# Kernel tuning notes

Hardware: AMD Instinct MI355X
Metric: run time of the kernel (lower is better)

The kernel has to match this reference:

```python
import jax, jax.numpy as jnp
import numpy as np

N = 50000
E = 800000
IN_C = 512
HID_C = 128
OUT_C = 16


def setup_inputs() -> dict:
    key = jax.random.key(0)
    k1, k2, k3, k4, k5 = jax.random.split(key, 5)
    x = jax.random.normal(k1, (N, IN_C), dtype=jnp.float32)
    edge_index = jax.random.randint(k2, (2, E), 0, N, dtype=jnp.int64)
    # GCNConv.lin: Linear(in, hid, bias=False); conv bias zero-init but give random for grad coverage
    W1 = jax.random.normal(k3, (HID_C, IN_C), dtype=jnp.float32) / np.sqrt(IN_C)
    b1 = jnp.zeros((HID_C,), dtype=jnp.float32)
    # GCNNet.fc: Linear(hid, out)
    W2 = jax.random.normal(k4, (OUT_C, HID_C), dtype=jnp.float32) / np.sqrt(HID_C)
    b2 = jax.random.normal(k5, (OUT_C,), dtype=jnp.float32) * 0.01
    return {"x": x, "edge_index": edge_index, "W1": W1, "b1": b1, "W2": W2, "b2": b2}


def reference(x, edge_index, W1, b1, W2, b2):
    # Dropout(p=0.5) is identity in eval mode.
    row, col = edge_index[0], edge_index[1]
    h = x @ W1.T                                    # [N, HID_C]
    deg = jax.ops.segment_sum(jnp.ones((E,), dtype=h.dtype), col, num_segments=N)
    # NOTE: source uses deg.pow(0.5) (sqrt, not inv-sqrt) — faithful to the code.
    d = jnp.sqrt(deg)
    norm = d[row] * d[col]                          # [E]
    msg = norm[:, None] * h[row]                    # gather + scale, [E, HID_C]
    agg = jax.ops.segment_sum(msg, col, num_segments=N)  # scatter-add, [N, HID_C]
    conv_out = agg + b1                             # [N, HID_C]
    return conv_out @ W2.T + b2                     # [N, OUT_C]
```

## Files before the change

kernel.cpp:

```cpp
#include <hip/hip_runtime.h>
#include <hip/hip_bf16.h>
#include <hip/hip_fp16.h>

#define IN_C 512
#define HID_C 128
#define OUT_C 16
#define STILE 8192
#define SSH  13
#define KCH_H 32

typedef float    f32x4 __attribute__((ext_vector_type(4)));
typedef float    f32x2 __attribute__((ext_vector_type(2)));
typedef int      i32x4 __attribute__((ext_vector_type(4)));
typedef _Float16 h16x2 __attribute__((ext_vector_type(2)));

__device__ inline void pk_atomic_add_f16(h16x2* addr, h16x2 val) {
#if __has_builtin(__builtin_amdgcn_global_atomic_fadd_v2f16)
    __builtin_amdgcn_global_atomic_fadd_v2f16(addr, val);
#else
    unsigned int* ap = (unsigned int*)addr;
    unsigned int old = *ap, assumed;
    do {
        assumed = old;
        h16x2 cur = __builtin_bit_cast(h16x2, assumed);
        h16x2 nv = cur + val;
        old = atomicCAS(ap, assumed, __builtin_bit_cast(unsigned int, nv));
    } while (old != assumed);
#endif
}

__global__ __launch_bounds__(256) void prep_hist_kernel(
        const float* __restrict__ W1, const float* __restrict__ b1,
        const float* __restrict__ W2, const float* __restrict__ b2,
        float* __restrict__ Wc, float* __restrict__ cconst,
        const int* __restrict__ ei, int* __restrict__ phist,
        unsigned int* __restrict__ agg32, int E, int nhist, int aggWords) {
    __shared__ int h[STILE];
    if (blockIdx.x < 32) {
        int idx = blockIdx.x * 256 + threadIdx.x;
        int o = idx >> 9;
        int k = idx & 511;
        float s = 0.f;
#pragma unroll 8
        for (int hh = 0; hh < HID_C; ++hh)
            s = fmaf(W2[o * HID_C + hh], W1[hh * IN_C + k], s);
        Wc[o * IN_C + k] = s;
        return;
    }
    if (blockIdx.x == 32) {
        if (threadIdx.x < OUT_C) {
            int o = threadIdx.x;
            float s = b2[o];
            for (int hh = 0; hh < HID_C; ++hh)
                s = fmaf(b1[hh], W2[o * HID_C + hh], s);
            cconst[o] = s;
        }
        return;
    }
    if (blockIdx.x >= 33 + nhist) {
        int i = (blockIdx.x - 33 - nhist) * 256 + threadIdx.x;
        if (i < aggWords) agg32[i] = 0u;
        return;
    }
    const int hb = blockIdx.x - 33;
    const int st = hb / KCH_H;
    const int k = hb - st * KCH_H;
    for (int i = threadIdx.x; i < STILE; i += 256) h[i] = 0;
    __syncthreads();

    const int chunk = (((E + KCH_H - 1) / KCH_H) + 3) & ~3;
    const int beg = k * chunk;
    const int end = min(E, beg + chunk);
    const int* cols = ei + E;

    const int nv = (end > beg) ? ((end - beg) >> 2) : 0;
    const i32x4* cv = (const i32x4*)(cols + beg);
    for (int i = threadIdx.x; i < nv; i += 256) {
        i32x4 c = cv[i];
#pragma unroll
        for (int j = 0; j < 4; ++j) {
            int cj = c[j];
            if ((cj >> SSH) == st) atomicAdd(&h[cj & (STILE - 1)], 1);
        }
    }
    for (int e = beg + (nv << 2) + threadIdx.x; e < end; e += 256) {
        int cj = cols[e];
        if ((cj >> SSH) == st) atomicAdd(&h[cj & (STILE - 1)], 1);
    }
    __syncthreads();
    int* outp = phist + (size_t)hb * STILE;
    for (int i = threadIdx.x; i < STILE; i += 256) outp[i] = h[i];
}

__global__ __launch_bounds__(256) void h2_kernel(const float* __restrict__ x,
                                                 const float* __restrict__ WcG,
                                                 const int* __restrict__ phist,
                                                 float* __restrict__ dsq,
                                                 _Float16* __restrict__ h2h, int N) {
    __shared__ float wl[16 * IN_C];
    for (int i = threadIdx.x; i < (16 * IN_C) / 4; i += 256)
        ((f32x4*)wl)[i] = ((const f32x4*)WcG)[i];
    __syncthreads();

    const int lane = threadIdx.x & 63;
    const int wid = (blockIdx.x * 256 + threadIdx.x) >> 6;
    const int nw  = (gridDim.x * 256) >> 6;

    for (int r0 = wid * 4; r0 < N; r0 += nw * 4) {
        const int rmax = min(4, N - r0);

        const int rr_d = lane >> 4;
        const int rd = min(r0 + rr_d, N - 1);
        const int std = rd >> SSH, id = rd & (STILE - 1);
        const int kd = lane & 15;
        const int* pb = phist + ((size_t)std * KCH_H) * STILE + id;
        int deg = pb[(size_t)kd * STILE] + pb[(size_t)(kd + 16) * STILE];
        deg += __shfl_xor(deg, 1, 64);
        deg += __shfl_xor(deg, 2, 64);
        deg += __shfl_xor(deg, 4, 64);
        deg += __shfl_xor(deg, 8, 64);
        const float dsq_r = sqrtf((float)deg);
        if (kd == 0 && rr_d < rmax) dsq[r0 + rr_d] = dsq_r;

        f32x4 a0[4], a1[4];
#pragma unroll
        for (int rr = 0; rr < 4; ++rr) {
            int r = r0 + (rr < rmax ? rr : 0);
            a0[rr] = *(const f32x4*)(x + (size_t)r * IN_C + 4 * lane);
            a1[rr] = *(const f32x4*)(x + (size_t)r * IN_C + 256 + 4 * lane);
        }
        float p[4][16];
#pragma unroll
        for (int oo = 0; oo < 16; ++oo) {
            f32x4 w0 = *(const f32x4*)(wl + oo * IN_C + 4 * lane);
            f32x4 w1 = *(const f32x4*)(wl + oo * IN_C + 256 + 4 * lane);
#pragma unroll
            for (int rr = 0; rr < 4; ++rr) {
                float s = a0[rr].x * w0.x;
                s = fmaf(a0[rr].y, w0.y, s);
                s = fmaf(a0[rr].z, w0.z, s);
                s = fmaf(a0[rr].w, w0.w, s);
                s = fmaf(a1[rr].x, w1.x, s);
                s = fmaf(a1[rr].y, w1.y, s);
                s = fmaf(a1[rr].z, w1.z, s);
                s = fmaf(a1[rr].w, w1.w, s);
                p[rr][oo] = s;
            }
        }
        float v[4];
#pragma unroll
        for (int rr = 0; rr < 4; ++rr) {
#define RSTEP(MASK, HALF)                                              \
            {                                                          \
                const bool hi = (lane & MASK) != 0;                    \
                _Pragma("unroll")                                      \
                for (int ii = 0; ii < HALF; ++ii) {                    \
                    float send = hi ? p[rr][ii] : p[rr][ii + HALF];    \
                    float recv = __shfl_xor(send, MASK, 64);           \
                    float keep = hi ? p[rr][ii + HALF] : p[rr][ii];    \
                    p[rr][ii] = keep + recv;                           \
                }                                                      \
            }
            RSTEP(1, 8)
            RSTEP(2, 4)
            RSTEP(4, 2)
            RSTEP(8, 1)
#undef RSTEP
            v[rr] = p[rr][0];
        }
        const bool h16 = (lane & 16) != 0;
        float sA = h16 ? v[0] : v[1];
        float mA = (h16 ? v[1] : v[0]) + __shfl_xor(sA, 16, 64);
        float sB = h16 ? v[2] : v[3];
        float mB = (h16 ? v[3] : v[2]) + __shfl_xor(sB, 16, 64);
        const bool h32 = (lane & 32) != 0;
        float sC = h32 ? mA : mB;
        float f  = (h32 ? mB : mA) + __shfl_xor(sC, 32, 64);
        const int qq = lane >> 4, jj = lane & 15;
        const int oo = ((jj & 1) << 3) | ((jj & 2) << 1) | ((jj & 4) >> 1) | ((jj & 8) >> 3);
        if (qq < rmax) {
            int r = r0 + qq;
            h2h[(size_t)r * OUT_C + oo] = (_Float16)(f * dsq_r);
        }
    }
}

__global__ __launch_bounds__(256) void edge_kernel(const int* __restrict__ ei,
                                                   const _Float16* __restrict__ h2h,
                                                   h16x2* __restrict__ agg, int E) {
    int t = blockIdx.x * 256 + threadIdx.x;
    int e = t >> 3;
    if (e >= E) return;
    int op = t & 7;
    int r = ei[e];
    int c = ei[E + e];
    h16x2 h = *(const h16x2*)(h2h + (size_t)r * OUT_C + (op << 1));
    pk_atomic_add_f16(&agg[(size_t)c * 8 + op], h);
}

__global__ void final_kernel(const h16x2* __restrict__ agg, const float* __restrict__ dsq,
                             const float* __restrict__ cconst, float* __restrict__ out,
                             int words) {
    int i = blockIdx.x * 256 + threadIdx.x;
    if (i >= words) return;
    int n = i >> 3;
    int o = (i & 7) << 1;
    h16x2 a = agg[i];
    float d = dsq[n];
    f32x2 r;
    r.x = fmaf(d, (float)a.x, cconst[o]);
    r.y = fmaf(d, (float)a.y, cconst[o + 1]);
    *(f32x2*)(out + ((size_t)i << 1)) = r;
}

extern "C" void kernel_launch(void* const* d_in, const int* in_sizes, int n_in,
                              void* d_out, int out_size, void* d_ws, size_t ws_size,
                              hipStream_t stream) {
    const float* x  = (const float*)d_in[0];
    const int*   ei = (const int*)d_in[1];
    const float* W1 = (const float*)d_in[2];
    const float* b1 = (const float*)d_in[3];
    const float* W2 = (const float*)d_in[4];
    const float* b2 = (const float*)d_in[5];
    float* out = (float*)d_out;

    const int N = in_sizes[0] / IN_C;
    const int E = in_sizes[1] / 2;
    const int ST = (N + STILE - 1) / STILE;
    const int nhist = ST * KCH_H;
    const int aggWords = (N * OUT_C) / 2;

    float* ws     = (float*)d_ws;
    float* Wc     = ws;
    float* cconst = ws + 16 * IN_C;
    float* dsq    = cconst + 16;
    _Float16* h2h = (_Float16*)(dsq + N);
    int*   phist  = (int*)((unsigned int*)(dsq + N) + 8 * (size_t)N);
    unsigned int* agg32 = (unsigned int*)(phist + (size_t)ST * KCH_H * STILE);
    h16x2* agg = (h16x2*)agg32;

    const int zblocks = (aggWords + 255) / 256;
    hipLaunchKernelGGL(prep_hist_kernel, dim3(33 + nhist + zblocks), dim3(256), 0, stream,
                       W1, b1, W2, b2, Wc, cconst, ei, phist, agg32, E, nhist, aggWords);
    hipLaunchKernelGGL(h2_kernel, dim3(1024), dim3(256), 0, stream, x, Wc, phist, dsq, h2h, N);
    hipLaunchKernelGGL(edge_kernel, dim3((E * 8 + 255) / 256), dim3(256), 0, stream,
                       ei, h2h, agg, E);
    hipLaunchKernelGGL(final_kernel, dim3((aggWords + 255) / 256), dim3(256), 0, stream,
                       agg, dsq, cconst, out, aggWords);
}
```

Measured before the change: 90.84 us.

## Software-pipeline x row loads in h2 kernel with two rows per wave iteration

The h2 projection kernel now processes two rows per wave iteration instead of four and prefetches the next iteration's x rows into registers while computing the current ones. The goal is to hide global-load latency on the memory-bound x stream through register double buffering. The degree lookup is restructured to one load per lane over 32 histogram chunks. Each iteration has less arithmetic per load and one extra shuffle stage, and the final store uses only half the lanes.

```diff
diff --git a/kernel.cpp b/kernel.cpp
--- a/kernel.cpp
+++ b/kernel.cpp
@@ -105,54 +105,79 @@
     const int lane = threadIdx.x & 63;
     const int wid = (blockIdx.x * 256 + threadIdx.x) >> 6;
     const int nw  = (gridDim.x * 256) >> 6;
-
-    for (int r0 = wid * 4; r0 < N; r0 += nw * 4) {
-        const int rmax = min(4, N - r0);
-
-        const int rr_d = lane >> 4;
+    const int stride = nw * 2;
+
+    int r0 = wid * 2;
+    if (r0 >= N) return;
+
+    f32x4 a0c0, a1c0, a0c1, a1c1;
+    {
+        int ra = r0, rb = min(r0 + 1, N - 1);
+        a0c0 = *(const f32x4*)(x + (size_t)ra * IN_C + 4 * lane);
+        a1c0 = *(const f32x4*)(x + (size_t)ra * IN_C + 256 + 4 * lane);
+        a0c1 = *(const f32x4*)(x + (size_t)rb * IN_C + 4 * lane);
+        a1c1 = *(const f32x4*)(x + (size_t)rb * IN_C + 256 + 4 * lane);
+    }
+
+    while (r0 < N) {
+        const int rnext = r0 + stride;
+        f32x4 a0n0, a1n0, a0n1, a1n1;
+        if (rnext < N) {
+            int ra = rnext, rb = min(rnext + 1, N - 1);
+            a0n0 = *(const f32x4*)(x + (size_t)ra * IN_C + 4 * lane);
+            a1n0 = *(const f32x4*)(x + (size_t)ra * IN_C + 256 + 4 * lane);
+            a0n1 = *(const f32x4*)(x + (size_t)rb * IN_C + 4 * lane);
+            a1n1 = *(const f32x4*)(x + (size_t)rb * IN_C + 256 + 4 * lane);
+        }
+        const int rmax = min(2, N - r0);
+
+        const int rr_d = lane >> 5;
         const int rd = min(r0 + rr_d, N - 1);
-        const int std = rd >> SSH, id = rd & (STILE - 1);
-        const int kd = lane & 15;
-        const int* pb = phist + ((size_t)std * KCH_H) * STILE + id;
-        int deg = pb[(size_t)kd * STILE] + pb[(size_t)(kd + 16) * STILE];
+        const int std_ = rd >> SSH, id_ = rd & (STILE - 1);
+        const int kd = lane & 31;
+        int deg = phist[((size_t)std_ * KCH_H + kd) * STILE + id_];
         deg += __shfl_xor(deg, 1, 64);
         deg += __shfl_xor(deg, 2, 64);
         deg += __shfl_xor(deg, 4, 64);
         deg += __shfl_xor(deg, 8, 64);
+        deg += __shfl_xor(deg, 16, 64);
         const float dsq_r = sqrtf((float)deg);
         if (kd == 0 && rr_d < rmax) dsq[r0 + rr_d] = dsq_r;
-
-        f32x4 a0[4], a1[4];
-#pragma unroll
-        for (int rr = 0; rr < 4; ++rr) {
-            int r = r0 + (rr < rmax ? rr : 0);
-            a0[rr] = *(const f32x4*)(x + (size_t)r * IN_C + 4 * lane);
-            a1[rr] = *(const f32x4*)(x + (size_t)r * IN_C + 256 + 4 * lane);
-        }
-        float p[4][16];
+        const float dsq_o = __shfl_xor(dsq_r, 32, 64);
+
+        float p[2][16];
 #pragma unroll
         for (int oo = 0; oo < 16; ++oo) {
             f32x4 w0 = *(const f32x4*)(wl + oo * IN_C + 4 * lane);
             f32x4 w1 = *(const f32x4*)(wl + oo * IN_C + 256 + 4 * lane);
-#pragma unroll
-            for (int rr = 0; rr < 4; ++rr) {
-                float s = a0[rr].x * w0.x;
-                s = fmaf(a0[rr].y, w0.y, s);
-                s = fmaf(a0[rr].z, w0.z, s);
-                s = fmaf(a0[rr].w, w0.w, s);
-                s = fmaf(a1[rr].x, w1.x, s);
-                s = fmaf(a1[rr].y, w1.y, s);
-                s = fmaf(a1[rr].z, w1.z, s);
-                s = fmaf(a1[rr].w, w1.w, s);
-                p[rr][oo] = s;
+            {
+                float s = a0c0.x * w0.x;
+                s = fmaf(a0c0.y, w0.y, s);
+                s = fmaf(a0c0.z, w0.z, s);
+                s = fmaf(a0c0.w, w0.w, s);
+                s = fmaf(a1c0.x, w1.x, s);
+                s = fmaf(a1c0.y, w1.y, s);
+                s = fmaf(a1c0.z, w1.z, s);
+                s = fmaf(a1c0.w, w1.w, s);
+                p[0][oo] = s;
             }
-        }
-        float v[4];
-#pragma unroll
-        for (int rr = 0; rr < 4; ++rr) {
+            {
+                float s = a0c1.x * w0.x;
+                s = fmaf(a0c1.y, w0.y, s);
+                s = fmaf(a0c1.z, w0.z, s);
+                s = fmaf(a0c1.w, w0.w, s);
+                s = fmaf(a1c1.x, w1.x, s);
+                s = fmaf(a1c1.y, w1.y, s);
+                s = fmaf(a1c1.z, w1.z, s);
+                s = fmaf(a1c1.w, w1.w, s);
+                p[1][oo] = s;
+            }
+        }
 #define RSTEP(MASK, HALF)                                              \
-            {                                                          \
-                const bool hi = (lane & MASK) != 0;                    \
+        {                                                              \
+            const bool hi = (lane & MASK) != 0;                        \
+            _Pragma("unroll")                                          \
+            for (int rr = 0; rr < 2; ++rr) {                           \
                 _Pragma("unroll")                                      \
                 for (int ii = 0; ii < HALF; ++ii) {                    \
                     float send = hi ? p[rr][ii] : p[rr][ii + HALF];    \
@@ -160,28 +185,29 @@
                     float keep = hi ? p[rr][ii + HALF] : p[rr][ii];    \
                     p[rr][ii] = keep + recv;                           \
                 }                                                      \
+            }                                                          \
+        }
+        RSTEP(1, 8)
+        RSTEP(2, 4)
+        RSTEP(4, 2)
+        RSTEP(8, 1)
+#undef RSTEP
+        const float v0 = p[0][0], v1 = p[1][0];
+        const bool h16 = (lane & 16) != 0;
+        float sA = h16 ? v0 : v1;
+        float mA = (h16 ? v1 : v0) + __shfl_xor(sA, 16, 64);
+        float f  = mA + __shfl_xor(mA, 32, 64);
+        if (lane < 32) {
+            int rsel = (lane >> 4) & 1;
+            if (rsel < rmax) {
+                const int jj = lane & 15;
+                const int oo = ((jj & 1) << 3) | ((jj & 2) << 1) | ((jj & 4) >> 1) | ((jj & 8) >> 3);
+                const float d = (lane & 16) ? dsq_o : dsq_r;
+                h2h[(size_t)(r0 + rsel) * OUT_C + oo] = (_Float16)(f * d);
             }
-            RSTEP(1, 8)
-            RSTEP(2, 4)
-            RSTEP(4, 2)
-            RSTEP(8, 1)
-#undef RSTEP
-            v[rr] = p[rr][0];
-        }
-        const bool h16 = (lane & 16) != 0;
-        float sA = h16 ? v[0] : v[1];
-        float mA = (h16 ? v[1] : v[0]) + __shfl_xor(sA, 16, 64);
-        float sB = h16 ? v[2] : v[3];
-        float mB = (h16 ? v[3] : v[2]) + __shfl_xor(sB, 16, 64);
-        const bool h32 = (lane & 32) != 0;
-        float sC = h32 ? mA : mB;
-        float f  = (h32 ? mB : mA) + __shfl_xor(sC, 32, 64);
-        const int qq = lane >> 4, jj = lane & 15;
-        const int oo = ((jj & 1) << 3) | ((jj & 2) << 1) | ((jj & 4) >> 1) | ((jj & 8) >> 3);
-        if (qq < rmax) {
-            int r = r0 + qq;
-            h2h[(size_t)r * OUT_C + oo] = (_Float16)(f * dsq_r);
-        }
+        }
+        r0 = rnext;
+        a0c0 = a0n0; a1c0 = a1n0; a0c1 = a0n1; a1c1 = a1n1;
     }
 }
 
```

After: 93.13 us. 2.5% more time.

## Replicate fp16 aggregation buffer across block groups to reduce atomic contention

Applied to the files above, without the earlier changes.

Splits the edge scatter-add across 8 replicated fp16 accumulation buffers, one per contiguous group of edge blocks, and sums the replicas in the final kernel. This aims to spread atomic traffic across more addresses and improve L2 atomic throughput, and it also keeps fp16 partial sums smaller, which may help precision. In exchange it costs 8x more zero-initialisation work and 8x more reads in the final kernel, plus a larger workspace. The h2 kernel grid is also halved.

```diff
diff --git a/kernel.cpp b/kernel.cpp
--- a/kernel.cpp
+++ b/kernel.cpp
@@ -8,6 +8,7 @@
 #define STILE 8192
 #define SSH  13
 #define KCH_H 32
+#define NREP 8
 
 typedef float    f32x4 __attribute__((ext_vector_type(4)));
 typedef float    f32x2 __attribute__((ext_vector_type(2)));
@@ -34,7 +35,7 @@
         const float* __restrict__ W2, const float* __restrict__ b2,
         float* __restrict__ Wc, float* __restrict__ cconst,
         const int* __restrict__ ei, int* __restrict__ phist,
-        unsigned int* __restrict__ agg32, int E, int nhist, int aggWords) {
+        unsigned int* __restrict__ agg32, int E, int nhist, int zeroWords) {
     __shared__ int h[STILE];
     if (blockIdx.x < 32) {
         int idx = blockIdx.x * 256 + threadIdx.x;
@@ -59,7 +60,7 @@
     }
     if (blockIdx.x >= 33 + nhist) {
         int i = (blockIdx.x - 33 - nhist) * 256 + threadIdx.x;
-        if (i < aggWords) agg32[i] = 0u;
+        if (i < zeroWords) agg32[i] = 0u;
         return;
     }
     const int hb = blockIdx.x - 33;
@@ -111,9 +112,9 @@
 
         const int rr_d = lane >> 4;
         const int rd = min(r0 + rr_d, N - 1);
-        const int std = rd >> SSH, id = rd & (STILE - 1);
+        const int std_ = rd >> SSH, id_ = rd & (STILE - 1);
         const int kd = lane & 15;
-        const int* pb = phist + ((size_t)std * KCH_H) * STILE + id;
+        const int* pb = phist + ((size_t)std_ * KCH_H) * STILE + id_;
         int deg = pb[(size_t)kd * STILE] + pb[(size_t)(kd + 16) * STILE];
         deg += __shfl_xor(deg, 1, 64);
         deg += __shfl_xor(deg, 2, 64);
@@ -187,7 +188,9 @@
 
 __global__ __launch_bounds__(256) void edge_kernel(const int* __restrict__ ei,
                                                    const _Float16* __restrict__ h2h,
-                                                   h16x2* __restrict__ agg, int E) {
+                                                   h16x2* __restrict__ agg,
+                                                   int E, int aggWords, int repDiv) {
+    h16x2* aggR = agg + (size_t)(blockIdx.x / repDiv) * aggWords;
     int t = blockIdx.x * 256 + threadIdx.x;
     int e = t >> 3;
     if (e >= E) return;
@@ -195,21 +198,27 @@
     int r = ei[e];
     int c = ei[E + e];
     h16x2 h = *(const h16x2*)(h2h + (size_t)r * OUT_C + (op << 1));
-    pk_atomic_add_f16(&agg[(size_t)c * 8 + op], h);
+    pk_atomic_add_f16(&aggR[(size_t)c * 8 + op], h);
 }
 
 __global__ void final_kernel(const h16x2* __restrict__ agg, const float* __restrict__ dsq,
                              const float* __restrict__ cconst, float* __restrict__ out,
-                             int words) {
+                             int words, int aggWords) {
     int i = blockIdx.x * 256 + threadIdx.x;
     if (i >= words) return;
     int n = i >> 3;
     int o = (i & 7) << 1;
-    h16x2 a = agg[i];
+    float sx = 0.f, sy = 0.f;
+#pragma unroll
+    for (int rep = 0; rep < NREP; ++rep) {
+        h16x2 a = agg[(size_t)rep * aggWords + i];
+        sx += (float)a.x;
+        sy += (float)a.y;
+    }
     float d = dsq[n];
     f32x2 r;
-    r.x = fmaf(d, (float)a.x, cconst[o]);
-    r.y = fmaf(d, (float)a.y, cconst[o + 1]);
+    r.x = fmaf(d, sx, cconst[o]);
+    r.y = fmaf(d, sy, cconst[o + 1]);
     *(f32x2*)(out + ((size_t)i << 1)) = r;
 }
 
@@ -229,6 +238,7 @@
     const int ST = (N + STILE - 1) / STILE;
     const int nhist = ST * KCH_H;
     const int aggWords = (N * OUT_C) / 2;
+    const int zeroWords = NREP * aggWords;
 
     float* ws     = (float*)d_ws;
     float* Wc     = ws;
@@ -239,12 +249,14 @@
     unsigned int* agg32 = (unsigned int*)(phist + (size_t)ST * KCH_H * STILE);
     h16x2* agg = (h16x2*)agg32;
 
-    const int zblocks = (aggWords + 255) / 256;
+    const int zblocks = (zeroWords + 255) / 256;
     hipLaunchKernelGGL(prep_hist_kernel, dim3(33 + nhist + zblocks), dim3(256), 0, stream,
-                       W1, b1, W2, b2, Wc, cconst, ei, phist, agg32, E, nhist, aggWords);
-    hipLaunchKernelGGL(h2_kernel, dim3(1024), dim3(256), 0, stream, x, Wc, phist, dsq, h2h, N);
-    hipLaunchKernelGGL(edge_kernel, dim3((E * 8 + 255) / 256), dim3(256), 0, stream,
-                       ei, h2h, agg, E);
+                       W1, b1, W2, b2, Wc, cconst, ei, phist, agg32, E, nhist, zeroWords);
+    hipLaunchKernelGGL(h2_kernel, dim3(512), dim3(256), 0, stream, x, Wc, phist, dsq, h2h, N);
+    const int eblocks = (E * 8 + 255) / 256;
+    const int repDiv = (eblocks + NREP - 1) / NREP;
+    hipLaunchKernelGGL(edge_kernel, dim3(eblocks), dim3(256), 0, stream,
+                       ei, h2h, agg, E, aggWords, repDiv);
     hipLaunchKernelGGL(final_kernel, dim3((aggWords + 255) / 256), dim3(256), 0, stream,
-                       agg, dsq, cconst, out, aggWords);
-}
+                       agg, dsq, cconst, out, aggWords, aggWords);
+}
```

Result: no change. 92.15 us (+1.4%).
